# Kernel tuning notes

Hardware: AMD Instinct MI355X
Metric: run time of the kernel (lower is better)

The kernel has to match this reference:

```python
import jax, jax.numpy as jnp
import numpy as np

S, B, E, H, V, L = 128, 64, 512, 1024, 10000, 2


def setup_inputs() -> dict:
    key = jax.random.key(0)
    ks = jax.random.split(key, 10)
    s = 0.02  # weight scale ~ uniform(-k,k) magnitude
    return {
        "inputs": jax.random.randint(ks[0], (S, B), 0, V),
        "hidden": jnp.zeros((L, B, H), jnp.float32),
        "emb": jax.random.normal(ks[1], (V, E), jnp.float32) * 0.1,
        "Wx0": jax.random.normal(ks[2], (3, H, E), jnp.float32) * s,
        "Uh0": jax.random.normal(ks[3], (3, H, H), jnp.float32) * s,
        "b0": jax.random.normal(ks[4], (3, H), jnp.float32) * s,
        "Wx1": jax.random.normal(ks[5], (3, H, H), jnp.float32) * s,
        "Uh1": jax.random.normal(ks[6], (3, H, H), jnp.float32) * s,
        "b1": jax.random.normal(ks[7], (3, H), jnp.float32) * s,
        "Wd": jax.random.normal(ks[8], (V, H), jnp.float32) * 0.1,
        "bd": jnp.zeros((V,), jnp.float32),
    }


def _gru_cell(xp, h, U, b):
    # xp: (3,B,H) precomputed input projections in [r,z,h] order
    r = jax.nn.sigmoid(xp[0] + h @ U[0].T + b[0])
    z = jax.nn.sigmoid(xp[1] + h @ U[1].T + b[1])
    h_tilde = jnp.tanh(xp[2] + (r * h) @ U[2].T + b[2])
    return (1.0 - z) * h + z * h_tilde


def reference(inputs, hidden, emb, Wx0, Uh0, b0, Wx1, Uh1, b1, Wd, bd):
    x_embs = emb[inputs]                                   # [S,B,E]
    # precompute layer-0 input projections across all timesteps
    xa0 = jnp.einsum("sbe,goe->sgbo", x_embs, Wx0)        # [S,3,B,H]

    def step(carry, xa0_t):
        h0, h1 = carry
        h0n = _gru_cell(xa0_t, h0, Uh0, b0)
        xp1 = jnp.einsum("bk,gok->gbo", h0n, Wx1)          # [3,B,H]
        h1n = _gru_cell(xp1, h1, Uh1, b1)
        return (h0n, h1n), h1n

    (h0f, h1f), hs1 = jax.lax.scan(step, (hidden[0], hidden[1]), xa0)
    logits = jnp.einsum("sbh,vh->sbv", hs1, Wd) + bd       # [S,B,V]
    return logits, jnp.stack([h0f, h1f])
```

## Files before the change

### kernel.cpp

```cpp
#include <hip/hip_runtime.h>
#include <hip/hip_bf16.h>

#define SLEN 128
#define BAT 64
#define EDIM 512
#define HDIM 1024
#define VOC 10000
#define VPAD 10112
#define NWG_REC 192
#define TPB_REC 512

typedef short v8s __attribute__((ext_vector_type(8)));
typedef float v4f __attribute__((ext_vector_type(4)));
typedef unsigned short u16;

__device__ __forceinline__ u16 f2bf(float f) {
  unsigned u = __float_as_uint(f);
  u += 0x7fffu + ((u >> 16) & 1u);
  return (u16)(u >> 16);
}
__device__ __forceinline__ float bf2f(u16 b) {
  return __uint_as_float(((unsigned)b) << 16);
}
__device__ __forceinline__ float sigm(float x) { return 1.f / (1.f + __expf(-x)); }
__device__ __forceinline__ float tanh_f(float x) { return 1.f - 2.f / (1.f + __expf(2.f * x)); }

__device__ __forceinline__ void st_f32(float* p, float v) {
  __hip_atomic_store(p, v, __ATOMIC_RELAXED, __HIP_MEMORY_SCOPE_AGENT);
}
__device__ __forceinline__ float ld_f32(const float* p) {
  return __hip_atomic_load(p, __ATOMIC_RELAXED, __HIP_MEMORY_SCOPE_AGENT);
}
__device__ __forceinline__ float ld_bf16(const unsigned* base, int elem) {
  unsigned pr = __hip_atomic_load(base + (elem >> 1), __ATOMIC_RELAXED, __HIP_MEMORY_SCOPE_AGENT);
  return bf2f((u16)((elem & 1) ? (pr >> 16) : (pr & 0xffffu)));
}
__device__ __forceinline__ void st_bf16_pair(unsigned* base, int elem, u16 val, int l) {
  unsigned p = (unsigned)__shfl_xor((int)val, 1);
  if ((l & 1) == 0)
    __hip_atomic_store(base + (elem >> 1), (unsigned)val | (p << 16),
                       __ATOMIC_RELAXED, __HIP_MEMORY_SCOPE_AGENT);
}

__device__ __forceinline__ void gbar(int* bar, int ph, int wg, int t) {
  asm volatile("s_waitcnt vmcnt(0) lgkmcnt(0)" ::: "memory");
  __syncthreads();
  if (t == 0)
    __hip_atomic_store(&bar[wg], ph, __ATOMIC_RELAXED, __HIP_MEMORY_SCOPE_AGENT);
  if (wg == 0) {
    if (t < 64) {
      for (;;) {
        int v0 = __hip_atomic_load(&bar[t],       __ATOMIC_RELAXED, __HIP_MEMORY_SCOPE_AGENT);
        int v1 = __hip_atomic_load(&bar[64 + t],  __ATOMIC_RELAXED, __HIP_MEMORY_SCOPE_AGENT);
        int v2 = __hip_atomic_load(&bar[128 + t], __ATOMIC_RELAXED, __HIP_MEMORY_SCOPE_AGENT);
        if (__all((v0 >= ph) & (v1 >= ph) & (v2 >= ph))) break;
        __builtin_amdgcn_s_sleep(1);
      }
      if (t == 0)
        __hip_atomic_store(&bar[256], ph, __ATOMIC_RELAXED, __HIP_MEMORY_SCOPE_AGENT);
    }
  } else if (t < 64) {
    while (__hip_atomic_load(&bar[256], __ATOMIC_RELAXED, __HIP_MEMORY_SCOPE_AGENT) < ph)
      __builtin_amdgcn_s_sleep(4);
  }
  __syncthreads();
}

__device__ __forceinline__ v4f gemm_sc(const char* apl, const char* bcl, int swz, int lk2) {
  v8s a[8];
  v4f acc0{0.f, 0.f, 0.f, 0.f}, acc1{0.f, 0.f, 0.f, 0.f};
#pragma unroll
  for (int j = 0; j < 8; ++j)
    asm volatile("global_load_dwordx4 %0, %1, off offset:%2 sc0 sc1"
                 : "=v"(a[j]) : "v"(apl), "i"(j * 64));
#pragma unroll
  for (int ks = 0; ks < 32; ++ks) {
    asm volatile("s_waitcnt vmcnt(%0)" :: "i"((ks < 24) ? 7 : (31 - ks)));
    __builtin_amdgcn_sched_barrier(0x3F6);
    v8s b = *(const v8s*)(bcl + ((ks * 64 + lk2) ^ swz));
    if (ks & 1) acc1 = __builtin_amdgcn_mfma_f32_16x16x32_bf16(a[ks & 7], b, acc1, 0, 0, 0);
    else        acc0 = __builtin_amdgcn_mfma_f32_16x16x32_bf16(a[ks & 7], b, acc0, 0, 0, 0);
    if (ks < 24)
      asm volatile("global_load_dwordx4 %0, %1, off offset:%2 sc0 sc1"
                   : "=v"(a[ks & 7]) : "v"(apl), "i"((ks + 8) * 64));
  }
  return acc0 + acc1;
}

__global__ void __launch_bounds__(512, 2) k_recur(
    const u16* __restrict__ Uh0b, const u16* __restrict__ Wx1b, const u16* __restrict__ Uh1b,
    const float* __restrict__ b0, const float* __restrict__ b1,
    const u16* __restrict__ xa0,
    float* __restrict__ h0f, u16* __restrict__ h0b,
    float* __restrict__ h1f, u16* __restrict__ h1b,
    u16* __restrict__ a2, float* __restrict__ z0,
    u16* __restrict__ a5, float* __restrict__ z1,
    u16* __restrict__ xp1,
    u16* __restrict__ hs1,
    float* __restrict__ outh,
    int* __restrict__ bar) {
  extern __shared__ char smem[];
  const int wg = blockIdx.x;
  const int t = threadIdx.x;
  const int w = t >> 6;
  const int l = t & 63;
  const int lr = l & 15;
  const int lk2 = (l >> 4) * 16;
  const int rg = w >> 1, cg = w & 1;
  const int rbase1 = rg * 16 + ((l >> 4) << 2);
  const int rbase2 = w * 16 + ((l >> 4) << 2);

  unsigned* a2u  = (unsigned*)a2;
  unsigned* a5u  = (unsigned*)a5;
  unsigned* h0bu = (unsigned*)h0b;
  unsigned* h1bu = (unsigned*)h1b;
  unsigned* xpu  = (unsigned*)xp1;

  {
    const u16* w1src; int w1row0;
    if (wg < 64)       { w1src = Uh0b; w1row0 = wg * 32; }
    else if (wg < 160) { w1src = Wx1b; w1row0 = (wg - 64) * 32; }
    else               { w1src = Uh1b; w1row0 = 2048 + (wg - 160) * 32; }
    const u16* w2src; int w2row0;
    if (wg < 64) { w2src = Uh0b; w2row0 = 2048 + wg * 16; }
    else         { w2src = Uh1b; w2row0 = (wg - 64) * 16; }
    for (int i = t; i < 4096; i += TPB_REC) {
      int c = i >> 7, j = i & 127;
      v8s v = *(const v8s*)(w1src + (size_t)(w1row0 + c) * HDIM + j * 8);
      int off = c * 2048 + ((j * 16) ^ ((c & 7) << 4));
      *(v8s*)(smem + off) = v;
    }
    for (int i = t; i < 2048; i += TPB_REC) {
      int c = i >> 7, j = i & 127;
      v8s v = *(const v8s*)(w2src + (size_t)(w2row0 + c) * HDIM + j * 8);
      int off = 65536 + c * 2048 + ((j * 16) ^ ((c & 7) << 4));
      *(v8s*)(smem + off) = v;
    }
    __syncthreads();
  }

  const char* bb1 = smem + (cg * 16 + lr) * 2048;
  const int swz1 = ((cg * 16 + lr) & 7) << 4;
  const char* bb2 = smem + 65536 + lr * 2048;
  const int swz2 = (lr & 7) << 4;

  for (int T = 0; T <= SLEN + 1; ++T) {
    if (wg < 64) {
      if (T < SLEN) {
        const int cglob = wg * 32 + cg * 16 + lr;
        const int g = cglob >> 10;
        const int o = cglob & 1023;
        const float bias = b0[g * HDIM + o];
        float xv[4], hv[4];
#pragma unroll
        for (int r = 0; r < 4; ++r) {
          int b = rbase1 + r;
          xv[r] = bf2f(xa0[((T * 3 + g) * BAT + b) * HDIM + o]);
          if (g == 0) hv[r] = ld_f32(&h0f[b * HDIM + o]);
        }
        const char* apl = (const char*)h0b + (rg * 16 + lr) * 2048 + lk2;
        v4f acc = gemm_sc(apl, bb1, swz1, lk2);
#pragma unroll
        for (int r = 0; r < 4; ++r) {
          int b = rbase1 + r;
          float s = sigm(acc[r] + xv[r] + bias);
          if (g == 0) st_bf16_pair(a2u, b * HDIM + o, f2bf(s * hv[r]), l);
          else        st_f32(&z0[b * HDIM + o], s);
        }
      }
    } else if (wg < 160) {
      if (T >= 1 && T <= SLEN) {
        const int n = (wg - 64) * 32 + cg * 16 + lr;
        const char* apl = (const char*)h0b + (rg * 16 + lr) * 2048 + lk2;
        v4f acc = gemm_sc(apl, bb1, swz1, lk2);
        unsigned* xp = xpu + (((T - 1) & 1) * (BAT * 3 * HDIM) >> 1);
#pragma unroll
        for (int r = 0; r < 4; ++r)
          st_bf16_pair(xp, (rbase1 + r) * 3072 + n, f2bf(acc[r]), l);
      }
    } else {
      if (T >= 2) {
        const int t5 = T - 2;
        const int o = (wg - 160) * 32 + cg * 16 + lr;
        const unsigned* xp = xpu + (((t5 & 1) * (BAT * 3 * HDIM)) >> 1);
        const float bias = b1[2 * HDIM + o];
        float xv[4], zv[4], hv[4];
#pragma unroll
        for (int r = 0; r < 4; ++r) {
          int b = rbase1 + r;
          xv[r] = ld_bf16(xp, b * 3072 + 2048 + o);
          zv[r] = ld_f32(&z1[b * HDIM + o]);
          hv[r] = ld_f32(&h1f[b * HDIM + o]);
        }
        const char* apl = (const char*)a5 + (rg * 16 + lr) * 2048 + lk2;
        v4f acc = gemm_sc(apl, bb1, swz1, lk2);
#pragma unroll
        for (int r = 0; r < 4; ++r) {
          int b = rbase1 + r;
          float ht = tanh_f(xv[r] + acc[r] + bias);
          float hn = (1.f - zv[r]) * hv[r] + zv[r] * ht;
          u16 hb = f2bf(hn);
          st_f32(&h1f[b * HDIM + o], hn);
          st_bf16_pair(h1bu, b * HDIM + o, hb, l);
          hs1[((size_t)t5 * BAT + b) * HDIM + o] = hb;
          if (t5 == SLEN - 1) outh[(size_t)BAT * HDIM + b * HDIM + o] = hn;
        }
      }
    }
    gbar(bar, 2 * T + 1, wg, t);
    if (w < 4) {
      if (wg < 64) {
        if (T < SLEN) {
          const int o = wg * 16 + lr;
          const float bias = b0[2 * HDIM + o];
          float xv[4], zv[4], hv[4];
#pragma unroll
          for (int r = 0; r < 4; ++r) {
            int b = rbase2 + r;
            xv[r] = bf2f(xa0[((T * 3 + 2) * BAT + b) * HDIM + o]);
            zv[r] = ld_f32(&z0[b * HDIM + o]);
            hv[r] = ld_f32(&h0f[b * HDIM + o]);
          }
          const char* apl = (const char*)a2 + (w * 16 + lr) * 2048 + lk2;
          v4f acc = gemm_sc(apl, bb2, swz2, lk2);
#pragma unroll
          for (int r = 0; r < 4; ++r) {
            int b = rbase2 + r;
            float ht = tanh_f(xv[r] + acc[r] + bias);
            float hn = (1.f - zv[r]) * hv[r] + zv[r] * ht;
            st_f32(&h0f[b * HDIM + o], hn);
            st_bf16_pair(h0bu, b * HDIM + o, f2bf(hn), l);
            if (T == SLEN - 1) outh[b * HDIM + o] = hn;
          }
        }
      } else {
        if (T >= 1 && T <= SLEN) {
          const int t4 = T - 1;
          const int cglob = (wg - 64) * 16 + lr;
          const int g = cglob >> 10;
          const int o = cglob & 1023;
          const unsigned* xp = xpu + (((t4 & 1) * (BAT * 3 * HDIM)) >> 1);
          const float bias = b1[g * HDIM + o];
          float xv[4], hv[4];
#pragma unroll
          for (int r = 0; r < 4; ++r) {
            int b = rbase2 + r;
            xv[r] = ld_bf16(xp, b * 3072 + g * HDIM + o);
            if (g == 0) hv[r] = ld_f32(&h1f[b * HDIM + o]);
          }
          const char* apl = (const char*)h1b + (w * 16 + lr) * 2048 + lk2;
          v4f acc = gemm_sc(apl, bb2, swz2, lk2);
#pragma unroll
          for (int r = 0; r < 4; ++r) {
            int b = rbase2 + r;
            float s = sigm(acc[r] + xv[r] + bias);
            if (g == 0) st_bf16_pair(a5u, b * HDIM + o, f2bf(s * hv[r]), l);
            else        st_f32(&z1[b * HDIM + o], s);
          }
        }
      }
    }
    gbar(bar, 2 * T + 2, wg, t);
  }
}

template <int MODE>
__global__ void __launch_bounds__(256) k_gemm(
    const u16* __restrict__ A, const u16* __restrict__ Bw,
    const int* __restrict__ gidx, const float* __restrict__ bias,
    void* __restrict__ Out) {
  constexpr int K = MODE ? 1024 : 512;
  constexpr int NB_N = MODE ? (VPAD / 128) : (3072 / 128);

  __shared__ u16 sA[128 * 64];
  __shared__ u16 sB[128 * 64];

  const int nwg = gridDim.x;
  const int cpx = nwg >> 3;
  const int bid = blockIdx.x;
  const int swz = (bid & 7) * cpx + (bid >> 3);
  const int bm = swz / NB_N, bn = swz % NB_N;
  const int m0 = bm * 128, n0 = bn * 128;

  const int t = threadIdx.x;
  const int w = t >> 6, l = t & 63;
  const int lr = l & 15, lk = (l >> 4) * 8;
  const int wm = (w >> 1) * 64, wn = (w & 1) * 64;
  const int kc = (t & 7) * 8;

  int arowg[4];
#pragma unroll
  for (int i = 0; i < 4; ++i) {
    int row = m0 + i * 32 + (t >> 3);
    arowg[i] = (MODE == 0) ? gidx[row] : row;
  }
  int brow[4];
#pragma unroll
  for (int i = 0; i < 4; ++i) brow[i] = n0 + i * 32 + (t >> 3);

  v4f acc[4][4];
#pragma unroll
  for (int mi = 0; mi < 4; ++mi)
#pragma unroll
    for (int ni = 0; ni < 4; ++ni) acc[mi][ni] = v4f{0.f, 0.f, 0.f, 0.f};

  for (int k0 = 0; k0 < K; k0 += 64) {
    __syncthreads();
#pragma unroll
    for (int i = 0; i < 4; ++i) {
      const u16* src = A + (size_t)arowg[i] * K + k0 + kc;
      __builtin_amdgcn_global_load_lds((const __attribute__((address_space(1))) void*)src,
                                       (__attribute__((address_space(3))) void*)(sA + i * 2048 + w * 512),
                                       16, 0, 0);
    }
#pragma unroll
    for (int i = 0; i < 4; ++i) {
      const u16* src = Bw + (size_t)brow[i] * K + k0 + kc;
      __builtin_amdgcn_global_load_lds((const __attribute__((address_space(1))) void*)src,
                                       (__attribute__((address_space(3))) void*)(sB + i * 2048 + w * 512),
                                       16, 0, 0);
    }
    asm volatile("s_waitcnt vmcnt(0)" ::: "memory");
    __syncthreads();
#pragma unroll
    for (int ks = 0; ks < 2; ++ks) {
      v8s af[4], bfr[4];
#pragma unroll
      for (int mi = 0; mi < 4; ++mi) af[mi] = *(const v8s*)&sA[(wm + mi * 16 + lr) * 64 + ks * 32 + lk];
#pragma unroll
      for (int ni = 0; ni < 4; ++ni) bfr[ni] = *(const v8s*)&sB[(wn + ni * 16 + lr) * 64 + ks * 32 + lk];
#pragma unroll
      for (int mi = 0; mi < 4; ++mi)
#pragma unroll
        for (int ni = 0; ni < 4; ++ni)
          acc[mi][ni] = __builtin_amdgcn_mfma_f32_16x16x32_bf16(af[mi], bfr[ni], acc[mi][ni], 0, 0, 0);
    }
  }

#pragma unroll
  for (int mi = 0; mi < 4; ++mi)
#pragma unroll
    for (int ni = 0; ni < 4; ++ni)
#pragma unroll
      for (int r = 0; r < 4; ++r) {
        int grow = m0 + wm + mi * 16 + ((l >> 4) << 2) + r;
        int gcol = n0 + wn + ni * 16 + lr;
        float v = acc[mi][ni][r];
        if (MODE == 0) {
          int s = grow >> 6, b = grow & 63;
          int g = gcol >> 10, o = gcol & 1023;
          ((u16*)Out)[(((size_t)s * 3 + g) * BAT + b) * HDIM + o] = f2bf(v);
        } else {
          if (gcol < VOC) ((float*)Out)[(size_t)grow * VOC + gcol] = v + bias[gcol];
        }
      }
}

__global__ void k_cvt(const float* __restrict__ src, u16* __restrict__ dst, int n, int nsrc) {
  int i = (blockIdx.x * 256 + threadIdx.x) * 4;
  if (i >= n) return;
#pragma unroll
  for (int j = 0; j < 4; ++j) {
    int idx = i + j;
    if (idx < n) dst[idx] = (idx < nsrc) ? f2bf(src[idx]) : (u16)0;
  }
}

__global__ void k_init(const float* __restrict__ hidden,
                       float* h0f, u16* h0b, float* h1f, u16* h1b, int* bar) {
  int i = blockIdx.x * 256 + threadIdx.x;
  if (i < BAT * HDIM) {
    float v0 = hidden[i];
    float v1 = hidden[BAT * HDIM + i];
    h0f[i] = v0; h0b[i] = f2bf(v0);
    h1f[i] = v1; h1b[i] = f2bf(v1);
  }
  if (i < 512) bar[i] = 0;
}

extern "C" void kernel_launch(void* const* d_in, const int* in_sizes, int n_in,
                              void* d_out, int out_size, void* d_ws, size_t ws_size,
                              hipStream_t stream) {
  const int*   inp = (const int*)d_in[0];
  const float* hid = (const float*)d_in[1];
  const float* emb = (const float*)d_in[2];
  const float* Wx0 = (const float*)d_in[3];
  const float* Uh0 = (const float*)d_in[4];
  const float* b0  = (const float*)d_in[5];
  const float* Wx1 = (const float*)d_in[6];
  const float* Uh1 = (const float*)d_in[7];
  const float* b1  = (const float*)d_in[8];
  const float* Wd  = (const float*)d_in[9];
  const float* bd  = (const float*)d_in[10];

  char* ws = (char*)d_ws;
  size_t off = 0;
  auto alloc = [&](size_t bytes) {
    void* p = ws + off;
    off = (off + bytes + 255) & ~(size_t)255;
    return p;
  };
  u16* emb_b = (u16*)alloc(sizeof(u16) * (size_t)VOC * EDIM);
  u16* Wx0_b = (u16*)alloc(sizeof(u16) * 3 * HDIM * EDIM);
  u16* Uh0_b = (u16*)alloc(sizeof(u16) * 3 * HDIM * HDIM);
  u16* Wx1_b = (u16*)alloc(sizeof(u16) * 3 * HDIM * HDIM);
  u16* Uh1_b = (u16*)alloc(sizeof(u16) * 3 * HDIM * HDIM);
  u16* Wd_b  = (u16*)alloc(sizeof(u16) * (size_t)VPAD * HDIM);
  u16* xa0_b = (u16*)alloc(sizeof(u16) * (size_t)SLEN * 3 * BAT * HDIM);
  u16* hs1_b = (u16*)alloc(sizeof(u16) * (size_t)SLEN * BAT * HDIM);
  u16* xp1   = (u16*)alloc(sizeof(u16) * 2 * BAT * 3 * HDIM);
  float* h0f = (float*)alloc(sizeof(float) * BAT * HDIM);
  float* h1f = (float*)alloc(sizeof(float) * BAT * HDIM);
  u16* h0b   = (u16*)alloc(sizeof(u16) * BAT * HDIM);
  u16* h1b   = (u16*)alloc(sizeof(u16) * BAT * HDIM);
  u16* a2    = (u16*)alloc(sizeof(u16) * BAT * HDIM);
  u16* a5    = (u16*)alloc(sizeof(u16) * BAT * HDIM);
  float* z0  = (float*)alloc(sizeof(float) * BAT * HDIM);
  float* z1  = (float*)alloc(sizeof(float) * BAT * HDIM);
  int* bar   = (int*)alloc(sizeof(int) * 512);

  float* logits = (float*)d_out;
  float* outh = logits + (size_t)SLEN * BAT * VOC;

  auto cvt = [&](const float* s, u16* d, int n, int nsrc) {
    k_cvt<<<dim3((n / 4 + 255) / 256), dim3(256), 0, stream>>>(s, d, n, nsrc);
  };
  cvt(emb, emb_b, VOC * EDIM, VOC * EDIM);
  cvt(Wx0, Wx0_b, 3 * HDIM * EDIM, 3 * HDIM * EDIM);
  cvt(Uh0, Uh0_b, 3 * HDIM * HDIM, 3 * HDIM * HDIM);
  cvt(Wx1, Wx1_b, 3 * HDIM * HDIM, 3 * HDIM * HDIM);
  cvt(Uh1, Uh1_b, 3 * HDIM * HDIM, 3 * HDIM * HDIM);
  cvt(Wd, Wd_b, VPAD * HDIM, VOC * HDIM);
  k_init<<<dim3(256), dim3(256), 0, stream>>>(hid, h0f, h0b, h1f, h1b, bar);

  k_gemm<0><<<dim3(64 * 24), dim3(256), 0, stream>>>(emb_b, Wx0_b, inp, (const float*)nullptr, (void*)xa0_b);

  (void)hipFuncSetAttribute(reinterpret_cast<const void*>(k_recur),
                            hipFuncAttributeMaxDynamicSharedMemorySize, 96 * 1024);
  k_recur<<<dim3(NWG_REC), dim3(TPB_REC), 96 * 1024, stream>>>(
      Uh0_b, Wx1_b, Uh1_b, b0, b1, xa0_b,
      h0f, h0b, h1f, h1b, a2, z0, a5, z1, xp1, hs1_b, outh, bar);

  k_gemm<1><<<dim3(64 * 79), dim3(256), 0, stream>>>(hs1_b, Wd_b, (const int*)nullptr, bd, d_out);
}
```

Measured before the change: 3.015 ms.

## Split recurrent kernel into producer/consumer groups with point-to-point flag sync

Replaces the centralized two-phase grid barrier with dedicated workgroup groups: 96 workgroups run phase-A work (r/z gates, Wx1 projection, layer-1 candidate) and 48 run phase-B work (layer-0 candidate, layer-1 r/z gates). Each group waits on per-workgroup flags published by the other group, removing the gather-then-broadcast barrier round trip. Workgroups grow to 1024 threads with 64 weight columns and 128KB of LDS each, so 144 workgroups replace 192. Unused flag slots are preset to a large value so the wave-wide polls pass. The phases can now overlap across groups, but each workgroup holds more work per step and occupancy drops to one workgroup per CU.

```diff
diff --git a/kernel.cpp b/kernel.cpp
--- a/kernel.cpp
+++ b/kernel.cpp
@@ -7,8 +7,8 @@
 #define HDIM 1024
 #define VOC 10000
 #define VPAD 10112
-#define NWG_REC 192
-#define TPB_REC 512
+#define NWG_REC 144
+#define TPB_REC 1024
 
 typedef short v8s __attribute__((ext_vector_type(8)));
 typedef float v4f __attribute__((ext_vector_type(4)));
@@ -40,30 +40,6 @@
   if ((l & 1) == 0)
     __hip_atomic_store(base + (elem >> 1), (unsigned)val | (p << 16),
                        __ATOMIC_RELAXED, __HIP_MEMORY_SCOPE_AGENT);
-}
-
-__device__ __forceinline__ void gbar(int* bar, int ph, int wg, int t) {
-  asm volatile("s_waitcnt vmcnt(0) lgkmcnt(0)" ::: "memory");
-  __syncthreads();
-  if (t == 0)
-    __hip_atomic_store(&bar[wg], ph, __ATOMIC_RELAXED, __HIP_MEMORY_SCOPE_AGENT);
-  if (wg == 0) {
-    if (t < 64) {
-      for (;;) {
-        int v0 = __hip_atomic_load(&bar[t],       __ATOMIC_RELAXED, __HIP_MEMORY_SCOPE_AGENT);
-        int v1 = __hip_atomic_load(&bar[64 + t],  __ATOMIC_RELAXED, __HIP_MEMORY_SCOPE_AGENT);
-        int v2 = __hip_atomic_load(&bar[128 + t], __ATOMIC_RELAXED, __HIP_MEMORY_SCOPE_AGENT);
-        if (__all((v0 >= ph) & (v1 >= ph) & (v2 >= ph))) break;
-        __builtin_amdgcn_s_sleep(1);
-      }
-      if (t == 0)
-        __hip_atomic_store(&bar[256], ph, __ATOMIC_RELAXED, __HIP_MEMORY_SCOPE_AGENT);
-    }
-  } else if (t < 64) {
-    while (__hip_atomic_load(&bar[256], __ATOMIC_RELAXED, __HIP_MEMORY_SCOPE_AGENT) < ph)
-      __builtin_amdgcn_s_sleep(4);
-  }
-  __syncthreads();
 }
 
 __device__ __forceinline__ v4f gemm_sc(const char* apl, const char* bcl, int swz, int lk2) {
@@ -87,7 +63,7 @@
   return acc0 + acc1;
 }
 
-__global__ void __launch_bounds__(512, 2) k_recur(
+__global__ void __launch_bounds__(TPB_REC) k_recur(
     const u16* __restrict__ Uh0b, const u16* __restrict__ Wx1b, const u16* __restrict__ Uh1b,
     const float* __restrict__ b0, const float* __restrict__ b1,
     const u16* __restrict__ xa0,
@@ -106,9 +82,11 @@
   const int l = t & 63;
   const int lr = l & 15;
   const int lk2 = (l >> 4) * 16;
-  const int rg = w >> 1, cg = w & 1;
-  const int rbase1 = rg * 16 + ((l >> 4) << 2);
-  const int rbase2 = w * 16 + ((l >> 4) << 2);
+  const int rowblk = (w >> 2) * 16;
+  const int colf = (w & 3) * 16 + lr;
+  const int rbase = rowblk + ((l >> 4) << 2);
+  const char* bb = smem + colf * 2048;
+  const int swz = (lr & 7) << 4;
 
   unsigned* a2u  = (unsigned*)a2;
   unsigned* a5u  = (unsigned*)a5;
@@ -117,115 +95,137 @@
   unsigned* xpu  = (unsigned*)xp1;
 
   {
-    const u16* w1src; int w1row0;
-    if (wg < 64)       { w1src = Uh0b; w1row0 = wg * 32; }
-    else if (wg < 160) { w1src = Wx1b; w1row0 = (wg - 64) * 32; }
-    else               { w1src = Uh1b; w1row0 = 2048 + (wg - 160) * 32; }
-    const u16* w2src; int w2row0;
-    if (wg < 64) { w2src = Uh0b; w2row0 = 2048 + wg * 16; }
-    else         { w2src = Uh1b; w2row0 = (wg - 64) * 16; }
-    for (int i = t; i < 4096; i += TPB_REC) {
+    const u16* wsrc; int wrow0;
+    if (wg < 32)       { wsrc = Uh0b; wrow0 = wg * 64; }
+    else if (wg < 80)  { wsrc = Wx1b; wrow0 = (wg - 32) * 64; }
+    else if (wg < 96)  { wsrc = Uh1b; wrow0 = 2048 + (wg - 80) * 64; }
+    else if (wg < 112) { wsrc = Uh0b; wrow0 = 2048 + (wg - 96) * 64; }
+    else               { wsrc = Uh1b; wrow0 = (wg - 112) * 64; }
+    for (int i = t; i < 8192; i += TPB_REC) {
       int c = i >> 7, j = i & 127;
-      v8s v = *(const v8s*)(w1src + (size_t)(w1row0 + c) * HDIM + j * 8);
-      int off = c * 2048 + ((j * 16) ^ ((c & 7) << 4));
-      *(v8s*)(smem + off) = v;
-    }
-    for (int i = t; i < 2048; i += TPB_REC) {
-      int c = i >> 7, j = i & 127;
-      v8s v = *(const v8s*)(w2src + (size_t)(w2row0 + c) * HDIM + j * 8);
-      int off = 65536 + c * 2048 + ((j * 16) ^ ((c & 7) << 4));
-      *(v8s*)(smem + off) = v;
+      v8s v = *(const v8s*)(wsrc + (size_t)(wrow0 + c) * HDIM + j * 8);
+      *(v8s*)(smem + c * 2048 + ((j * 16) ^ ((c & 7) << 4))) = v;
     }
     __syncthreads();
   }
 
-  const char* bb1 = smem + (cg * 16 + lr) * 2048;
-  const int swz1 = ((cg * 16 + lr) & 7) << 4;
-  const char* bb2 = smem + 65536 + lr * 2048;
-  const int swz2 = (lr & 7) << 4;
-
-  for (int T = 0; T <= SLEN + 1; ++T) {
-    if (wg < 64) {
-      if (T < SLEN) {
-        const int cglob = wg * 32 + cg * 16 + lr;
-        const int g = cglob >> 10;
-        const int o = cglob & 1023;
-        const float bias = b0[g * HDIM + o];
-        float xv[4], hv[4];
-#pragma unroll
-        for (int r = 0; r < 4; ++r) {
-          int b = rbase1 + r;
-          xv[r] = bf2f(xa0[((T * 3 + g) * BAT + b) * HDIM + o]);
-          if (g == 0) hv[r] = ld_f32(&h0f[b * HDIM + o]);
-        }
-        const char* apl = (const char*)h0b + (rg * 16 + lr) * 2048 + lk2;
-        v4f acc = gemm_sc(apl, bb1, swz1, lk2);
-#pragma unroll
-        for (int r = 0; r < 4; ++r) {
-          int b = rbase1 + r;
-          float s = sigm(acc[r] + xv[r] + bias);
-          if (g == 0) st_bf16_pair(a2u, b * HDIM + o, f2bf(s * hv[r]), l);
-          else        st_f32(&z0[b * HDIM + o], s);
-        }
-      }
-    } else if (wg < 160) {
-      if (T >= 1 && T <= SLEN) {
-        const int n = (wg - 64) * 32 + cg * 16 + lr;
-        const char* apl = (const char*)h0b + (rg * 16 + lr) * 2048 + lk2;
-        v4f acc = gemm_sc(apl, bb1, swz1, lk2);
-        unsigned* xp = xpu + (((T - 1) & 1) * (BAT * 3 * HDIM) >> 1);
+  if (wg < 96) {
+    const int grp = (wg < 32) ? 0 : (wg < 80) ? 1 : 2;
+    for (int T = 0; T <= SLEN + 1; ++T) {
+      float xv[4];
+      if (grp == 0 && T < SLEN) {
+        const int g = wg >> 4;
+        const int o = (wg * 64 + colf) & 1023;
 #pragma unroll
         for (int r = 0; r < 4; ++r)
-          st_bf16_pair(xp, (rbase1 + r) * 3072 + n, f2bf(acc[r]), l);
-      }
-    } else {
-      if (T >= 2) {
-        const int t5 = T - 2;
-        const int o = (wg - 160) * 32 + cg * 16 + lr;
-        const unsigned* xp = xpu + (((t5 & 1) * (BAT * 3 * HDIM)) >> 1);
-        const float bias = b1[2 * HDIM + o];
-        float xv[4], zv[4], hv[4];
-#pragma unroll
-        for (int r = 0; r < 4; ++r) {
-          int b = rbase1 + r;
-          xv[r] = ld_bf16(xp, b * 3072 + 2048 + o);
-          zv[r] = ld_f32(&z1[b * HDIM + o]);
-          hv[r] = ld_f32(&h1f[b * HDIM + o]);
-        }
-        const char* apl = (const char*)a5 + (rg * 16 + lr) * 2048 + lk2;
-        v4f acc = gemm_sc(apl, bb1, swz1, lk2);
-#pragma unroll
-        for (int r = 0; r < 4; ++r) {
-          int b = rbase1 + r;
-          float ht = tanh_f(xv[r] + acc[r] + bias);
-          float hn = (1.f - zv[r]) * hv[r] + zv[r] * ht;
-          u16 hb = f2bf(hn);
-          st_f32(&h1f[b * HDIM + o], hn);
-          st_bf16_pair(h1bu, b * HDIM + o, hb, l);
-          hs1[((size_t)t5 * BAT + b) * HDIM + o] = hb;
-          if (t5 == SLEN - 1) outh[(size_t)BAT * HDIM + b * HDIM + o] = hn;
-        }
-      }
-    }
-    gbar(bar, 2 * T + 1, wg, t);
-    if (w < 4) {
-      if (wg < 64) {
+          xv[r] = bf2f(xa0[((T * 3 + g) * BAT + rbase + r) * HDIM + o]);
+      }
+      if (T >= 1) {
+        if (t < 64) {
+          for (;;) {
+            int v = __hip_atomic_load(&bar[128 + t], __ATOMIC_RELAXED, __HIP_MEMORY_SCOPE_AGENT);
+            if (__all(v >= T)) break;
+            __builtin_amdgcn_s_sleep(1);
+          }
+        }
+        __syncthreads();
+      }
+      if (grp == 0) {
         if (T < SLEN) {
-          const int o = wg * 16 + lr;
+          const int g = wg >> 4;
+          const int o = (wg * 64 + colf) & 1023;
+          const float bias = b0[g * HDIM + o];
+          float hv[4];
+          if (g == 0)
+#pragma unroll
+            for (int r = 0; r < 4; ++r) hv[r] = ld_f32(&h0f[(rbase + r) * HDIM + o]);
+          const char* apl = (const char*)h0b + (rowblk + lr) * 2048 + lk2;
+          v4f acc = gemm_sc(apl, bb, swz, lk2);
+#pragma unroll
+          for (int r = 0; r < 4; ++r) {
+            float s = sigm(acc[r] + xv[r] + bias);
+            if (g == 0) st_bf16_pair(a2u, (rbase + r) * HDIM + o, f2bf(s * hv[r]), l);
+            else        st_f32(&z0[(rbase + r) * HDIM + o], s);
+          }
+        }
+      } else if (grp == 1) {
+        if (T >= 1 && T <= SLEN) {
+          const int n = (wg - 32) * 64 + colf;
+          const char* apl = (const char*)h0b + (rowblk + lr) * 2048 + lk2;
+          v4f acc = gemm_sc(apl, bb, swz, lk2);
+          unsigned* xp = xpu + ((((T - 1) & 1) * (BAT * 3 * HDIM)) >> 1);
+#pragma unroll
+          for (int r = 0; r < 4; ++r)
+            st_bf16_pair(xp, (rbase + r) * 3072 + n, f2bf(acc[r]), l);
+        }
+      } else {
+        if (T >= 2) {
+          const int t5 = T - 2;
+          const int o = (wg - 80) * 64 + colf;
+          const unsigned* xp = xpu + (((t5 & 1) * (BAT * 3 * HDIM)) >> 1);
+          const float bias = b1[2 * HDIM + o];
+          float pv[4], zv[4], hv[4];
+#pragma unroll
+          for (int r = 0; r < 4; ++r) {
+            int b = rbase + r;
+            pv[r] = ld_bf16(xp, b * 3072 + 2048 + o);
+            zv[r] = ld_f32(&z1[b * HDIM + o]);
+            hv[r] = ld_f32(&h1f[b * HDIM + o]);
+          }
+          const char* apl = (const char*)a5 + (rowblk + lr) * 2048 + lk2;
+          v4f acc = gemm_sc(apl, bb, swz, lk2);
+#pragma unroll
+          for (int r = 0; r < 4; ++r) {
+            int b = rbase + r;
+            float ht = tanh_f(pv[r] + acc[r] + bias);
+            float hn = (1.f - zv[r]) * hv[r] + zv[r] * ht;
+            u16 hb = f2bf(hn);
+            st_f32(&h1f[b * HDIM + o], hn);
+            st_bf16_pair(h1bu, b * HDIM + o, hb, l);
+            hs1[((size_t)t5 * BAT + b) * HDIM + o] = hb;
+            if (t5 == SLEN - 1) outh[(size_t)BAT * HDIM + b * HDIM + o] = hn;
+          }
+        }
+      }
+      asm volatile("s_waitcnt vmcnt(0) lgkmcnt(0)" ::: "memory");
+      __syncthreads();
+      if (t == 0)
+        __hip_atomic_store(&bar[wg], T + 1, __ATOMIC_RELAXED, __HIP_MEMORY_SCOPE_AGENT);
+    }
+  } else {
+    for (int T = 0; T <= SLEN; ++T) {
+      float xv[4];
+      if (wg < 112 && T < SLEN) {
+        const int o = (wg - 96) * 64 + colf;
+#pragma unroll
+        for (int r = 0; r < 4; ++r)
+          xv[r] = bf2f(xa0[((T * 3 + 2) * BAT + rbase + r) * HDIM + o]);
+      }
+      if (t < 64) {
+        for (;;) {
+          int v0 = __hip_atomic_load(&bar[t],      __ATOMIC_RELAXED, __HIP_MEMORY_SCOPE_AGENT);
+          int v1 = __hip_atomic_load(&bar[64 + t], __ATOMIC_RELAXED, __HIP_MEMORY_SCOPE_AGENT);
+          if (__all((v0 >= T + 1) & (v1 >= T + 1))) break;
+          __builtin_amdgcn_s_sleep(1);
+        }
+      }
+      __syncthreads();
+      if (wg < 112) {
+        if (T < SLEN) {
+          const int o = (wg - 96) * 64 + colf;
           const float bias = b0[2 * HDIM + o];
-          float xv[4], zv[4], hv[4];
-#pragma unroll
-          for (int r = 0; r < 4; ++r) {
-            int b = rbase2 + r;
-            xv[r] = bf2f(xa0[((T * 3 + 2) * BAT + b) * HDIM + o]);
+          float zv[4], hv[4];
+#pragma unroll
+          for (int r = 0; r < 4; ++r) {
+            int b = rbase + r;
             zv[r] = ld_f32(&z0[b * HDIM + o]);
             hv[r] = ld_f32(&h0f[b * HDIM + o]);
           }
-          const char* apl = (const char*)a2 + (w * 16 + lr) * 2048 + lk2;
-          v4f acc = gemm_sc(apl, bb2, swz2, lk2);
-#pragma unroll
-          for (int r = 0; r < 4; ++r) {
-            int b = rbase2 + r;
+          const char* apl = (const char*)a2 + (rowblk + lr) * 2048 + lk2;
+          v4f acc = gemm_sc(apl, bb, swz, lk2);
+#pragma unroll
+          for (int r = 0; r < 4; ++r) {
+            int b = rbase + r;
             float ht = tanh_f(xv[r] + acc[r] + bias);
             float hn = (1.f - zv[r]) * hv[r] + zv[r] * ht;
             st_f32(&h0f[b * HDIM + o], hn);
@@ -234,33 +234,35 @@
           }
         }
       } else {
-        if (T >= 1 && T <= SLEN) {
+        if (T >= 1) {
           const int t4 = T - 1;
-          const int cglob = (wg - 64) * 16 + lr;
-          const int g = cglob >> 10;
-          const int o = cglob & 1023;
+          const int g = (wg - 112) >> 4;
+          const int o = ((wg - 112) * 64 + colf) & 1023;
           const unsigned* xp = xpu + (((t4 & 1) * (BAT * 3 * HDIM)) >> 1);
           const float bias = b1[g * HDIM + o];
-          float xv[4], hv[4];
-#pragma unroll
-          for (int r = 0; r < 4; ++r) {
-            int b = rbase2 + r;
-            xv[r] = ld_bf16(xp, b * 3072 + g * HDIM + o);
+          float pv[4], hv[4];
+#pragma unroll
+          for (int r = 0; r < 4; ++r) {
+            int b = rbase + r;
+            pv[r] = ld_bf16(xp, b * 3072 + g * HDIM + o);
             if (g == 0) hv[r] = ld_f32(&h1f[b * HDIM + o]);
           }
-          const char* apl = (const char*)h1b + (w * 16 + lr) * 2048 + lk2;
-          v4f acc = gemm_sc(apl, bb2, swz2, lk2);
-#pragma unroll
-          for (int r = 0; r < 4; ++r) {
-            int b = rbase2 + r;
-            float s = sigm(acc[r] + xv[r] + bias);
+          const char* apl = (const char*)h1b + (rowblk + lr) * 2048 + lk2;
+          v4f acc = gemm_sc(apl, bb, swz, lk2);
+#pragma unroll
+          for (int r = 0; r < 4; ++r) {
+            int b = rbase + r;
+            float s = sigm(acc[r] + pv[r] + bias);
             if (g == 0) st_bf16_pair(a5u, b * HDIM + o, f2bf(s * hv[r]), l);
             else        st_f32(&z1[b * HDIM + o], s);
           }
         }
       }
-    }
-    gbar(bar, 2 * T + 2, wg, t);
+      asm volatile("s_waitcnt vmcnt(0) lgkmcnt(0)" ::: "memory");
+      __syncthreads();
+      if (t == 0)
+        __hip_atomic_store(&bar[128 + (wg - 96)], T + 1, __ATOMIC_RELAXED, __HIP_MEMORY_SCOPE_AGENT);
+    }
   }
 }
 
@@ -375,7 +377,8 @@
     h0f[i] = v0; h0b[i] = f2bf(v0);
     h1f[i] = v1; h1b[i] = f2bf(v1);
   }
-  if (i < 512) bar[i] = 0;
+  if (i < 512)
+    bar[i] = ((i >= 96 && i < 128) || (i >= 176)) ? 0x7fffffff : 0;
 }
 
 extern "C" void kernel_launch(void* const* d_in, const int* in_sizes, int n_in,
@@ -436,8 +439,8 @@
   k_gemm<0><<<dim3(64 * 24), dim3(256), 0, stream>>>(emb_b, Wx0_b, inp, (const float*)nullptr, (void*)xa0_b);
 
   (void)hipFuncSetAttribute(reinterpret_cast<const void*>(k_recur),
-                            hipFuncAttributeMaxDynamicSharedMemorySize, 96 * 1024);
-  k_recur<<<dim3(NWG_REC), dim3(TPB_REC), 96 * 1024, stream>>>(
+                            hipFuncAttributeMaxDynamicSharedMemorySize, 128 * 1024);
+  k_recur<<<dim3(NWG_REC), dim3(TPB_REC), 128 * 1024, stream>>>(
       Uh0_b, Wx1_b, Uh1_b, b0, b1, xa0_b,
       h0f, h0b, h1f, h1b, a2, z0, a5, z1, xp1, hs1_b, outh, bar);
 
```

Result: slower. 6.388 ms (+111.9%).

## Split-K recurrent GEMMs across wave pairs and rebalance phase-2 work

Applied to the files above, without the earlier changes.

Each wave pair now splits the K dimension of the recurrent GEMMs in half, computes two 16-column fragments per wave, and reduces the partial sums through shared memory. Phase-2 work moves from half the waves in every workgroup to all waves in 96 workgroups, so no waves sit idle during that phase. The goal is a shorter per-step critical path in the latency-bound recurrence. In exchange it adds an LDS reduction plus a syncthreads per GEMM and raises dynamic shared memory to 136KB, which may limit occupancy to one workgroup per CU.

```diff
diff --git a/kernel.cpp b/kernel.cpp
--- a/kernel.cpp
+++ b/kernel.cpp
@@ -66,28 +66,51 @@
   __syncthreads();
 }
 
-__device__ __forceinline__ v4f gemm_sc(const char* apl, const char* bcl, int swz, int lk2) {
+__device__ __forceinline__ void gemm32p(const char* apl, const char* bcl,
+                                        int swz, int lk2, int kbase,
+                                        v4f& acc0, v4f& acc1) {
   v8s a[8];
-  v4f acc0{0.f, 0.f, 0.f, 0.f}, acc1{0.f, 0.f, 0.f, 0.f};
 #pragma unroll
   for (int j = 0; j < 8; ++j)
     asm volatile("global_load_dwordx4 %0, %1, off offset:%2 sc0 sc1"
                  : "=v"(a[j]) : "v"(apl), "i"(j * 64));
 #pragma unroll
-  for (int ks = 0; ks < 32; ++ks) {
-    asm volatile("s_waitcnt vmcnt(%0)" :: "i"((ks < 24) ? 7 : (31 - ks)));
+  for (int ks = 0; ks < 16; ++ks) {
+    asm volatile("s_waitcnt vmcnt(%0)" :: "i"((ks < 8) ? 7 : (15 - ks)));
     __builtin_amdgcn_sched_barrier(0x3F6);
-    v8s b = *(const v8s*)(bcl + ((ks * 64 + lk2) ^ swz));
-    if (ks & 1) acc1 = __builtin_amdgcn_mfma_f32_16x16x32_bf16(a[ks & 7], b, acc1, 0, 0, 0);
-    else        acc0 = __builtin_amdgcn_mfma_f32_16x16x32_bf16(a[ks & 7], b, acc0, 0, 0, 0);
-    if (ks < 24)
+    const int off = (kbase + ks * 64 + lk2) ^ swz;
+    v8s b0 = *(const v8s*)(bcl + off);
+    v8s b1 = *(const v8s*)(bcl + 32768 + off);
+    acc0 = __builtin_amdgcn_mfma_f32_16x16x32_bf16(a[ks & 7], b0, acc0, 0, 0, 0);
+    acc1 = __builtin_amdgcn_mfma_f32_16x16x32_bf16(a[ks & 7], b1, acc1, 0, 0, 0);
+    if (ks < 8)
       asm volatile("global_load_dwordx4 %0, %1, off offset:%2 sc0 sc1"
                    : "=v"(a[ks & 7]) : "v"(apl), "i"((ks + 8) * 64));
   }
-  return acc0 + acc1;
-}
-
-__global__ void __launch_bounds__(512, 2) k_recur(
+}
+
+__device__ __forceinline__ void reduce2(char* smem, int rg, int kg, int l,
+                                        v4f& acc0, v4f& acc1) {
+  float* scr = (float*)(smem + 131072);
+  const int base = rg * 512 + ((l >> 4) << 2) * 32 + (l & 15);
+  if (kg) {
+#pragma unroll
+    for (int r = 0; r < 4; ++r) {
+      scr[base + r * 32]      = acc0[r];
+      scr[base + r * 32 + 16] = acc1[r];
+    }
+  }
+  __syncthreads();
+  if (!kg) {
+#pragma unroll
+    for (int r = 0; r < 4; ++r) {
+      acc0[r] += scr[base + r * 32];
+      acc1[r] += scr[base + r * 32 + 16];
+    }
+  }
+}
+
+__global__ void __launch_bounds__(TPB_REC, 2) k_recur(
     const u16* __restrict__ Uh0b, const u16* __restrict__ Wx1b, const u16* __restrict__ Uh1b,
     const float* __restrict__ b0, const float* __restrict__ b1,
     const u16* __restrict__ xa0,
@@ -106,9 +129,10 @@
   const int l = t & 63;
   const int lr = l & 15;
   const int lk2 = (l >> 4) * 16;
-  const int rg = w >> 1, cg = w & 1;
-  const int rbase1 = rg * 16 + ((l >> 4) << 2);
-  const int rbase2 = w * 16 + ((l >> 4) << 2);
+  const int rg = w >> 1;
+  const int kg = w & 1;
+  const int rbase = rg * 16 + ((l >> 4) << 2);
+  const int swz = (lr & 7) << 4;
 
   unsigned* a2u  = (unsigned*)a2;
   unsigned* a5u  = (unsigned*)a5;
@@ -121,141 +145,199 @@
     if (wg < 64)       { w1src = Uh0b; w1row0 = wg * 32; }
     else if (wg < 160) { w1src = Wx1b; w1row0 = (wg - 64) * 32; }
     else               { w1src = Uh1b; w1row0 = 2048 + (wg - 160) * 32; }
-    const u16* w2src; int w2row0;
-    if (wg < 64) { w2src = Uh0b; w2row0 = 2048 + wg * 16; }
-    else         { w2src = Uh1b; w2row0 = (wg - 64) * 16; }
     for (int i = t; i < 4096; i += TPB_REC) {
       int c = i >> 7, j = i & 127;
       v8s v = *(const v8s*)(w1src + (size_t)(w1row0 + c) * HDIM + j * 8);
-      int off = c * 2048 + ((j * 16) ^ ((c & 7) << 4));
-      *(v8s*)(smem + off) = v;
-    }
-    for (int i = t; i < 2048; i += TPB_REC) {
-      int c = i >> 7, j = i & 127;
-      v8s v = *(const v8s*)(w2src + (size_t)(w2row0 + c) * HDIM + j * 8);
-      int off = 65536 + c * 2048 + ((j * 16) ^ ((c & 7) << 4));
-      *(v8s*)(smem + off) = v;
+      *(v8s*)(smem + c * 2048 + ((j * 16) ^ ((c & 7) << 4))) = v;
+    }
+    if (wg < 96) {
+      const u16* w2src; int w2row0;
+      if (wg < 32) { w2src = Uh0b; w2row0 = 2048 + wg * 32; }
+      else         { w2src = Uh1b; w2row0 = (wg - 32) * 32; }
+      for (int i = t; i < 4096; i += TPB_REC) {
+        int c = i >> 7, j = i & 127;
+        v8s v = *(const v8s*)(w2src + (size_t)(w2row0 + c) * HDIM + j * 8);
+        *(v8s*)(smem + 65536 + c * 2048 + ((j * 16) ^ ((c & 7) << 4))) = v;
+      }
     }
     __syncthreads();
   }
 
-  const char* bb1 = smem + (cg * 16 + lr) * 2048;
-  const int swz1 = ((cg * 16 + lr) & 7) << 4;
+  const char* bb1 = smem + lr * 2048;
   const char* bb2 = smem + 65536 + lr * 2048;
-  const int swz2 = (lr & 7) << 4;
+  const int kb = kg * 1024;
 
   for (int T = 0; T <= SLEN + 1; ++T) {
     if (wg < 64) {
       if (T < SLEN) {
-        const int cglob = wg * 32 + cg * 16 + lr;
-        const int g = cglob >> 10;
-        const int o = cglob & 1023;
-        const float bias = b0[g * HDIM + o];
-        float xv[4], hv[4];
-#pragma unroll
-        for (int r = 0; r < 4; ++r) {
-          int b = rbase1 + r;
-          xv[r] = bf2f(xa0[((T * 3 + g) * BAT + b) * HDIM + o]);
-          if (g == 0) hv[r] = ld_f32(&h0f[b * HDIM + o]);
-        }
-        const char* apl = (const char*)h0b + (rg * 16 + lr) * 2048 + lk2;
-        v4f acc = gemm_sc(apl, bb1, swz1, lk2);
-#pragma unroll
-        for (int r = 0; r < 4; ++r) {
-          int b = rbase1 + r;
-          float s = sigm(acc[r] + xv[r] + bias);
-          if (g == 0) st_bf16_pair(a2u, b * HDIM + o, f2bf(s * hv[r]), l);
-          else        st_f32(&z0[b * HDIM + o], s);
+        const int g = wg >> 5;
+        v4f acc0{0.f,0.f,0.f,0.f}, acc1{0.f,0.f,0.f,0.f};
+        float xv[2][4], hv[2][4];
+        if (!kg) {
+#pragma unroll
+          for (int fc = 0; fc < 2; ++fc) {
+            const int o = (wg * 32 + fc * 16 + lr) & 1023;
+#pragma unroll
+            for (int r = 0; r < 4; ++r) {
+              xv[fc][r] = bf2f(xa0[((T * 3 + g) * BAT + rbase + r) * HDIM + o]);
+              if (g == 0) hv[fc][r] = ld_f32(&h0f[(rbase + r) * HDIM + o]);
+            }
+          }
+        }
+        const char* apl = (const char*)h0b + (rg * 16 + lr) * 2048 + kb + lk2;
+        gemm32p(apl, bb1, swz, lk2, kb, acc0, acc1);
+        reduce2(smem, rg, kg, l, acc0, acc1);
+        if (!kg) {
+#pragma unroll
+          for (int fc = 0; fc < 2; ++fc) {
+            const int o = (wg * 32 + fc * 16 + lr) & 1023;
+            const float bias = b0[g * HDIM + o];
+            v4f& acc = fc ? acc1 : acc0;
+#pragma unroll
+            for (int r = 0; r < 4; ++r) {
+              int b = rbase + r;
+              float s = sigm(acc[r] + xv[fc][r] + bias);
+              if (g == 0) st_bf16_pair(a2u, b * HDIM + o, f2bf(s * hv[fc][r]), l);
+              else        st_f32(&z0[b * HDIM + o], s);
+            }
+          }
         }
       }
     } else if (wg < 160) {
       if (T >= 1 && T <= SLEN) {
-        const int n = (wg - 64) * 32 + cg * 16 + lr;
-        const char* apl = (const char*)h0b + (rg * 16 + lr) * 2048 + lk2;
-        v4f acc = gemm_sc(apl, bb1, swz1, lk2);
-        unsigned* xp = xpu + (((T - 1) & 1) * (BAT * 3 * HDIM) >> 1);
-#pragma unroll
-        for (int r = 0; r < 4; ++r)
-          st_bf16_pair(xp, (rbase1 + r) * 3072 + n, f2bf(acc[r]), l);
+        v4f acc0{0.f,0.f,0.f,0.f}, acc1{0.f,0.f,0.f,0.f};
+        const char* apl = (const char*)h0b + (rg * 16 + lr) * 2048 + kb + lk2;
+        gemm32p(apl, bb1, swz, lk2, kb, acc0, acc1);
+        reduce2(smem, rg, kg, l, acc0, acc1);
+        if (!kg) {
+          unsigned* xp = xpu + ((((T - 1) & 1) * (BAT * 3 * HDIM)) >> 1);
+#pragma unroll
+          for (int fc = 0; fc < 2; ++fc) {
+            const int n = (wg - 64) * 32 + fc * 16 + lr;
+            v4f& acc = fc ? acc1 : acc0;
+#pragma unroll
+            for (int r = 0; r < 4; ++r)
+              st_bf16_pair(xp, (rbase + r) * 3072 + n, f2bf(acc[r]), l);
+          }
+        }
       }
     } else {
       if (T >= 2) {
         const int t5 = T - 2;
-        const int o = (wg - 160) * 32 + cg * 16 + lr;
         const unsigned* xp = xpu + (((t5 & 1) * (BAT * 3 * HDIM)) >> 1);
-        const float bias = b1[2 * HDIM + o];
-        float xv[4], zv[4], hv[4];
-#pragma unroll
-        for (int r = 0; r < 4; ++r) {
-          int b = rbase1 + r;
-          xv[r] = ld_bf16(xp, b * 3072 + 2048 + o);
-          zv[r] = ld_f32(&z1[b * HDIM + o]);
-          hv[r] = ld_f32(&h1f[b * HDIM + o]);
-        }
-        const char* apl = (const char*)a5 + (rg * 16 + lr) * 2048 + lk2;
-        v4f acc = gemm_sc(apl, bb1, swz1, lk2);
-#pragma unroll
-        for (int r = 0; r < 4; ++r) {
-          int b = rbase1 + r;
-          float ht = tanh_f(xv[r] + acc[r] + bias);
-          float hn = (1.f - zv[r]) * hv[r] + zv[r] * ht;
-          u16 hb = f2bf(hn);
-          st_f32(&h1f[b * HDIM + o], hn);
-          st_bf16_pair(h1bu, b * HDIM + o, hb, l);
-          hs1[((size_t)t5 * BAT + b) * HDIM + o] = hb;
-          if (t5 == SLEN - 1) outh[(size_t)BAT * HDIM + b * HDIM + o] = hn;
+        v4f acc0{0.f,0.f,0.f,0.f}, acc1{0.f,0.f,0.f,0.f};
+        float pv[2][4], zv[2][4], hv[2][4];
+        if (!kg) {
+#pragma unroll
+          for (int fc = 0; fc < 2; ++fc) {
+            const int o = (wg - 160) * 32 + fc * 16 + lr;
+#pragma unroll
+            for (int r = 0; r < 4; ++r) {
+              int b = rbase + r;
+              pv[fc][r] = ld_bf16(xp, b * 3072 + 2048 + o);
+              zv[fc][r] = ld_f32(&z1[b * HDIM + o]);
+              hv[fc][r] = ld_f32(&h1f[b * HDIM + o]);
+            }
+          }
+        }
+        const char* apl = (const char*)a5 + (rg * 16 + lr) * 2048 + kb + lk2;
+        gemm32p(apl, bb1, swz, lk2, kb, acc0, acc1);
+        reduce2(smem, rg, kg, l, acc0, acc1);
+        if (!kg) {
+#pragma unroll
+          for (int fc = 0; fc < 2; ++fc) {
+            const int o = (wg - 160) * 32 + fc * 16 + lr;
+            const float bias = b1[2 * HDIM + o];
+            v4f& acc = fc ? acc1 : acc0;
+#pragma unroll
+            for (int r = 0; r < 4; ++r) {
+              int b = rbase + r;
+              float ht = tanh_f(pv[fc][r] + acc[r] + bias);
+              float hn = (1.f - zv[fc][r]) * hv[fc][r] + zv[fc][r] * ht;
+              u16 hb = f2bf(hn);
+              st_f32(&h1f[b * HDIM + o], hn);
+              st_bf16_pair(h1bu, b * HDIM + o, hb, l);
+              hs1[((size_t)t5 * BAT + b) * HDIM + o] = hb;
+              if (t5 == SLEN - 1) outh[(size_t)BAT * HDIM + b * HDIM + o] = hn;
+            }
+          }
         }
       }
     }
     gbar(bar, 2 * T + 1, wg, t);
-    if (w < 4) {
-      if (wg < 64) {
-        if (T < SLEN) {
-          const int o = wg * 16 + lr;
-          const float bias = b0[2 * HDIM + o];
-          float xv[4], zv[4], hv[4];
-#pragma unroll
-          for (int r = 0; r < 4; ++r) {
-            int b = rbase2 + r;
-            xv[r] = bf2f(xa0[((T * 3 + 2) * BAT + b) * HDIM + o]);
-            zv[r] = ld_f32(&z0[b * HDIM + o]);
-            hv[r] = ld_f32(&h0f[b * HDIM + o]);
-          }
-          const char* apl = (const char*)a2 + (w * 16 + lr) * 2048 + lk2;
-          v4f acc = gemm_sc(apl, bb2, swz2, lk2);
-#pragma unroll
-          for (int r = 0; r < 4; ++r) {
-            int b = rbase2 + r;
-            float ht = tanh_f(xv[r] + acc[r] + bias);
-            float hn = (1.f - zv[r]) * hv[r] + zv[r] * ht;
-            st_f32(&h0f[b * HDIM + o], hn);
-            st_bf16_pair(h0bu, b * HDIM + o, f2bf(hn), l);
-            if (T == SLEN - 1) outh[b * HDIM + o] = hn;
-          }
-        }
-      } else {
-        if (T >= 1 && T <= SLEN) {
-          const int t4 = T - 1;
-          const int cglob = (wg - 64) * 16 + lr;
-          const int g = cglob >> 10;
-          const int o = cglob & 1023;
-          const unsigned* xp = xpu + (((t4 & 1) * (BAT * 3 * HDIM)) >> 1);
-          const float bias = b1[g * HDIM + o];
-          float xv[4], hv[4];
-#pragma unroll
-          for (int r = 0; r < 4; ++r) {
-            int b = rbase2 + r;
-            xv[r] = ld_bf16(xp, b * 3072 + g * HDIM + o);
-            if (g == 0) hv[r] = ld_f32(&h1f[b * HDIM + o]);
-          }
-          const char* apl = (const char*)h1b + (w * 16 + lr) * 2048 + lk2;
-          v4f acc = gemm_sc(apl, bb2, swz2, lk2);
-#pragma unroll
-          for (int r = 0; r < 4; ++r) {
-            int b = rbase2 + r;
-            float s = sigm(acc[r] + xv[r] + bias);
-            if (g == 0) st_bf16_pair(a5u, b * HDIM + o, f2bf(s * hv[r]), l);
-            else        st_f32(&z1[b * HDIM + o], s);
+    if (wg < 32) {
+      if (T < SLEN) {
+        v4f acc0{0.f,0.f,0.f,0.f}, acc1{0.f,0.f,0.f,0.f};
+        float xv[2][4], zv[2][4], hv[2][4];
+        if (!kg) {
+#pragma unroll
+          for (int fc = 0; fc < 2; ++fc) {
+            const int o = wg * 32 + fc * 16 + lr;
+#pragma unroll
+            for (int r = 0; r < 4; ++r) {
+              int b = rbase + r;
+              xv[fc][r] = bf2f(xa0[((T * 3 + 2) * BAT + b) * HDIM + o]);
+              zv[fc][r] = ld_f32(&z0[b * HDIM + o]);
+              hv[fc][r] = ld_f32(&h0f[b * HDIM + o]);
+            }
+          }
+        }
+        const char* apl = (const char*)a2 + (rg * 16 + lr) * 2048 + kb + lk2;
+        gemm32p(apl, bb2, swz, lk2, kb, acc0, acc1);
+        reduce2(smem, rg, kg, l, acc0, acc1);
+        if (!kg) {
+#pragma unroll
+          for (int fc = 0; fc < 2; ++fc) {
+            const int o = wg * 32 + fc * 16 + lr;
+            const float bias = b0[2 * HDIM + o];
+            v4f& acc = fc ? acc1 : acc0;
+#pragma unroll
+            for (int r = 0; r < 4; ++r) {
+              int b = rbase + r;
+              float ht = tanh_f(xv[fc][r] + acc[r] + bias);
+              float hn = (1.f - zv[fc][r]) * hv[fc][r] + zv[fc][r] * ht;
+              st_f32(&h0f[b * HDIM + o], hn);
+              st_bf16_pair(h0bu, b * HDIM + o, f2bf(hn), l);
+              if (T == SLEN - 1) outh[b * HDIM + o] = hn;
+            }
+          }
+        }
+      }
+    } else if (wg < 96) {
+      if (T >= 1 && T <= SLEN) {
+        const int t4 = T - 1;
+        const int g = (wg - 32) >> 5;
+        const unsigned* xp = xpu + (((t4 & 1) * (BAT * 3 * HDIM)) >> 1);
+        v4f acc0{0.f,0.f,0.f,0.f}, acc1{0.f,0.f,0.f,0.f};
+        float pv[2][4], hv[2][4];
+        if (!kg) {
+#pragma unroll
+          for (int fc = 0; fc < 2; ++fc) {
+            const int o = ((wg - 32) * 32 + fc * 16 + lr) & 1023;
+#pragma unroll
+            for (int r = 0; r < 4; ++r) {
+              int b = rbase + r;
+              pv[fc][r] = ld_bf16(xp, b * 3072 + g * HDIM + o);
+              if (g == 0) hv[fc][r] = ld_f32(&h1f[b * HDIM + o]);
+            }
+          }
+        }
+        const char* apl = (const char*)h1b + (rg * 16 + lr) * 2048 + kb + lk2;
+        gemm32p(apl, bb2, swz, lk2, kb, acc0, acc1);
+        reduce2(smem, rg, kg, l, acc0, acc1);
+        if (!kg) {
+#pragma unroll
+          for (int fc = 0; fc < 2; ++fc) {
+            const int o = ((wg - 32) * 32 + fc * 16 + lr) & 1023;
+            const float bias = b1[g * HDIM + o];
+            v4f& acc = fc ? acc1 : acc0;
+#pragma unroll
+            for (int r = 0; r < 4; ++r) {
+              int b = rbase + r;
+              float s = sigm(acc[r] + pv[fc][r] + bias);
+              if (g == 0) st_bf16_pair(a5u, b * HDIM + o, f2bf(s * hv[fc][r]), l);
+              else        st_f32(&z1[b * HDIM + o], s);
+            }
           }
         }
       }
@@ -436,8 +518,8 @@
   k_gemm<0><<<dim3(64 * 24), dim3(256), 0, stream>>>(emb_b, Wx0_b, inp, (const float*)nullptr, (void*)xa0_b);
 
   (void)hipFuncSetAttribute(reinterpret_cast<const void*>(k_recur),
-                            hipFuncAttributeMaxDynamicSharedMemorySize, 96 * 1024);
-  k_recur<<<dim3(NWG_REC), dim3(TPB_REC), 96 * 1024, stream>>>(
+                            hipFuncAttributeMaxDynamicSharedMemorySize, 139264);
+  k_recur<<<dim3(NWG_REC), dim3(TPB_REC), 139264, stream>>>(
       Uh0_b, Wx1_b, Uh1_b, b0, b1, xa0_b,
       h0f, h0b, h1f, h1b, a2, z0, a5, z1, xp1, hs1_b, outh, bar);
 
```

Measured after the change: 3.943 ms. 1.31x slower.
